# Performance work log

Hardware: AMD Instinct MI355X
Metric: run time of the kernel (lower is better)

The kernel has to match this reference:

```python
import jax, jax.numpy as jnp
from jax import lax
import numpy as np

T = 140
H = 64
B = 8192

def _uniform(key, shape, k):
    return jax.random.uniform(key, shape, dtype=jnp.float32, minval=-k, maxval=k)

def setup_inputs() -> dict:
    key = jax.random.key(0)
    ks = jax.random.split(key, 12)
    k = 1.0 / np.sqrt(H)  # torch default init bound
    return {
        "x": jax.random.normal(ks[0], (B, T, 1), dtype=jnp.float32),
        "h_state": jnp.zeros((2, B, H), dtype=jnp.float32),
        "W_ih0": _uniform(ks[1], (H, 1), k),
        "W_hh0": _uniform(ks[2], (H, H), k),
        "b_ih0": _uniform(ks[3], (H,), k),
        "b_hh0": _uniform(ks[4], (H,), k),
        "W_ih1": _uniform(ks[5], (H, H), k),
        "W_hh1": _uniform(ks[6], (H, H), k),
        "b_ih1": _uniform(ks[7], (H,), k),
        "b_hh1": _uniform(ks[8], (H,), k),
        "W_out": _uniform(ks[9], (1, H), k),
        "b_out": _uniform(ks[10], (1,), k),
    }

def reference(x, h_state, W_ih0, W_hh0, b_ih0, b_hh0, W_ih1, W_hh1, b_ih1, b_hh1, W_out, b_out):
    b = x.shape[0]
    x = x.reshape(b, T, 1)
    xs = jnp.swapaxes(x, 0, 1)  # [T, B, 1]

    def step(carry, xt):
        h0, h1 = carry
        # torch RNN cell: h_t = tanh(x W_ih^T + b_ih + h_{t-1} W_hh^T + b_hh)
        h0n = jnp.tanh(xt @ W_ih0.T + b_ih0 + h0 @ W_hh0.T + b_hh0)
        h1n = jnp.tanh(h0n @ W_ih1.T + b_ih1 + h1 @ W_hh1.T + b_hh1)
        return (h0n, h1n), h1n

    (hf0, hf1), ys = lax.scan(step, (h_state[0], h_state[1]), xs)
    ys = jnp.swapaxes(ys, 0, 1)  # [B, T, H]
    out = (ys @ W_out.T + b_out).reshape(b, T, 1)
    h_final = jnp.stack([hf0, hf1])  # [2, B, H]
    return out, h_final
```

## Files before the change

kernel.cpp:

```cpp
#include <hip/hip_runtime.h>

#define TT 140
#define BB 8192
#define HH 64
#define BT 16
#define WIN 4
#define K_TANH 2.88539008178f

typedef _Float16 half4 __attribute__((ext_vector_type(4)));
typedef float    f32x4 __attribute__((ext_vector_type(4)));

#define MFMA16(a,b,c) __builtin_amdgcn_mfma_f32_16x16x16f16(a, b, c, 0, 0, 0)

__device__ __forceinline__ float tanh_ps(float as) {
    float e = __builtin_amdgcn_exp2f(as);
    return 1.0f - 2.0f * __builtin_amdgcn_rcpf(e + 1.0f);
}

__device__ __forceinline__ half4 ldw4(const float* p, float s) {
    f32x4 w = *(const f32x4*)p;
    half4 h;
    #pragma unroll
    for (int i = 0; i < 4; ++i) h[i] = (_Float16)(s * w[i]);
    return h;
}

__global__ __launch_bounds__(128, 1)
void rnn_kernel(const float* __restrict__ x,
                const float* __restrict__ h_state,
                const float* __restrict__ W_ih0,
                const float* __restrict__ W_hh0,
                const float* __restrict__ b_ih0,
                const float* __restrict__ b_hh0,
                const float* __restrict__ W_ih1,
                const float* __restrict__ W_hh1,
                const float* __restrict__ b_ih1,
                const float* __restrict__ b_hh1,
                const float* __restrict__ W_out,
                const float* __restrict__ b_out,
                float* __restrict__ out)
{
    __shared__ float xs[TT * 17];
    __shared__ float pps[TT * 17];
    __shared__ f32x4 ei[2 * WIN][4][64];

    const int tid  = threadIdx.x;
    const int wid  = tid >> 6;
    const int lane = tid & 63;
    const int n    = lane & 15;
    const int q    = lane >> 4;
    const int b0   = blockIdx.x * BT;

    half4 A0[4][4], AI[4][4], AH[4][4];
    float e00[4][4], e10[4][4], e01[4][4], WO[4][4];
    half4 H0[4], H1[4];
    float bout = 0.f;
    if (wid == 0) {
        #pragma unroll
        for (int g = 0; g < 4; ++g)
        #pragma unroll
        for (int kk = 0; kk < 4; ++kk) {
            const int off = (16 * g + n) * HH + 16 * kk + 4 * q;
            A0[g][kk] = ldw4(W_hh0 + off, K_TANH);
            AI[g][kk] = ldw4(W_ih1 + off, K_TANH);
        }
        #pragma unroll
        for (int g = 0; g < 4; ++g)
        #pragma unroll
        for (int r = 0; r < 4; ++r) {
            int j = 16 * g + 4 * q + r;
            e00[g][r] = K_TANH * (b_ih0[j] + b_hh0[j]);
            e10[g][r] = K_TANH * W_ih0[j];
        }
        #pragma unroll
        for (int kk = 0; kk < 4; ++kk)
            H0[kk] = ldw4(h_state + (size_t)(b0 + n) * HH + 16 * kk + 4 * q, 1.0f);
    } else {
        #pragma unroll
        for (int g = 0; g < 4; ++g)
        #pragma unroll
        for (int kk = 0; kk < 4; ++kk) {
            const int off = (16 * g + n) * HH + 16 * kk + 4 * q;
            AH[g][kk] = ldw4(W_hh1 + off, K_TANH);
        }
        #pragma unroll
        for (int g = 0; g < 4; ++g)
        #pragma unroll
        for (int r = 0; r < 4; ++r) {
            int j = 16 * g + 4 * q + r;
            e01[g][r] = K_TANH * (b_ih1[j] + b_hh1[j]);
            WO[g][r]  = W_out[j];
        }
        #pragma unroll
        for (int kk = 0; kk < 4; ++kk)
            H1[kk] = ldw4(h_state + (size_t)BB * HH + (size_t)(b0 + n) * HH
                                   + 16 * kk + 4 * q, 1.0f);
        bout = b_out[0];
    }

    for (int i = tid; i < TT * BT; i += 128) {
        int t = i >> 4, b = i & 15;
        xs[t * 17 + b] = x[(size_t)(b0 + b) * TT + t];
    }
    __syncthreads();

    for (int win = 0; win <= TT / WIN; ++win) {
        if (wid == 0) {
            if (win < TT / WIN) {
                #pragma unroll
                for (int j = 0; j < WIN; ++j) {
                    const int p  = WIN * win + j;
                    const int pb = ((win & 1) ? WIN : 0) + j;
                    float xt = xs[p * 17 + n];
                    f32x4 d[4];
                    #pragma unroll
                    for (int g = 0; g < 4; ++g) {
                        f32x4 c;
                        #pragma unroll
                        for (int r = 0; r < 4; ++r) c[r] = e00[g][r] + e10[g][r] * xt;
                        #pragma unroll
                        for (int kk = 0; kk < 4; ++kk) c = MFMA16(A0[g][kk], H0[kk], c);
                        d[g] = c;
                    }
                    #pragma unroll
                    for (int g = 0; g < 4; ++g) {
                        half4 h;
                        #pragma unroll
                        for (int r = 0; r < 4; ++r) h[r] = (_Float16)tanh_ps(d[g][r]);
                        H0[g] = h;
                    }
                    #pragma unroll
                    for (int g = 0; g < 4; ++g) {
                        f32x4 c = {0.f, 0.f, 0.f, 0.f};
                        #pragma unroll
                        for (int kk = 0; kk < 4; ++kk) c = MFMA16(AI[g][kk], H0[kk], c);
                        ei[pb][g][lane] = c;
                    }
                }
            }
        } else {
            if (win >= 1) {
                #pragma unroll
                for (int j = 0; j < WIN; ++j) {
                    const int s  = WIN * (win - 1) + j;
                    const int sb = (((win - 1) & 1) ? WIN : 0) + j;
                    f32x4 d[4];
                    #pragma unroll
                    for (int g = 0; g < 4; ++g) {
                        f32x4 ep = ei[sb][g][lane];
                        f32x4 c;
                        #pragma unroll
                        for (int r = 0; r < 4; ++r) c[r] = e01[g][r] + ep[r];
                        #pragma unroll
                        for (int kk = 0; kk < 4; ++kk) c = MFMA16(AH[g][kk], H1[kk], c);
                        d[g] = c;
                    }
                    float pr = 0.f;
                    #pragma unroll
                    for (int g = 0; g < 4; ++g) {
                        half4 h;
                        #pragma unroll
                        for (int r = 0; r < 4; ++r) {
                            float hn = tanh_ps(d[g][r]);
                            pr += hn * WO[g][r];
                            h[r] = (_Float16)hn;
                        }
                        H1[g] = h;
                    }
                    pr += __shfl_xor(pr, 16, 64);
                    pr += __shfl_xor(pr, 32, 64);
                    if (lane < 16) pps[s * 17 + n] = pr + bout;
                }
            }
        }
        __syncthreads();
    }

    for (int i = tid; i < TT * BT; i += 128) {
        int t = i >> 4, b = i & 15;
        out[(size_t)(b0 + b) * TT + t] = pps[t * 17 + b];
    }
    const size_t OFF = (size_t)BB * TT;
    if (wid == 0) {
        #pragma unroll
        for (int kk = 0; kk < 4; ++kk) {
            f32x4 v;
            #pragma unroll
            for (int i = 0; i < 4; ++i) v[i] = (float)H0[kk][i];
            *(f32x4*)(out + OFF + (size_t)(b0 + n) * HH + 16 * kk + 4 * q) = v;
        }
    } else {
        #pragma unroll
        for (int kk = 0; kk < 4; ++kk) {
            f32x4 v;
            #pragma unroll
            for (int i = 0; i < 4; ++i) v[i] = (float)H1[kk][i];
            *(f32x4*)(out + OFF + (size_t)BB * HH + (size_t)(b0 + n) * HH
                               + 16 * kk + 4 * q) = v;
        }
    }
}

extern "C" void kernel_launch(void* const* d_in, const int* in_sizes, int n_in,
                              void* d_out, int out_size, void* d_ws, size_t ws_size,
                              hipStream_t stream) {
    const float* x      = (const float*)d_in[0];
    const float* hst    = (const float*)d_in[1];
    const float* W_ih0  = (const float*)d_in[2];
    const float* W_hh0  = (const float*)d_in[3];
    const float* b_ih0  = (const float*)d_in[4];
    const float* b_hh0  = (const float*)d_in[5];
    const float* W_ih1  = (const float*)d_in[6];
    const float* W_hh1  = (const float*)d_in[7];
    const float* b_ih1  = (const float*)d_in[8];
    const float* b_hh1  = (const float*)d_in[9];
    const float* W_out  = (const float*)d_in[10];
    const float* b_outp = (const float*)d_in[11];
    float* out = (float*)d_out;

    dim3 grid(BB / BT);
    dim3 block(128);
    rnn_kernel<<<grid, block, 0, stream>>>(x, hst, W_ih0, W_hh0, b_ih0, b_hh0,
                                           W_ih1, W_hh1, b_ih1, b_hh1,
                                           W_out, b_outp, out);
}
```

Before: 170.8 us.

## Switch recurrent matmuls to 16x16x32 f16 MFMA with bpermute state redistribution

Replaces the 16x16x16 f16 MFMA chains (four per output group) with the 16x16x32 instruction available on this architecture, halving the number of MFMA issues per step. Because the K=32 operand layout no longer matches the accumulator layout, the new hidden state is packed to half2 and reshuffled across lanes with ds_bpermute before the next step. This trades serial MFMA latency on the recurrence critical path for extra cross-lane permute traffic.

```diff
diff --git a/kernel.cpp b/kernel.cpp
--- a/kernel.cpp
+++ b/kernel.cpp
@@ -7,22 +7,53 @@
 #define WIN 4
 #define K_TANH 2.88539008178f
 
-typedef _Float16 half4 __attribute__((ext_vector_type(4)));
-typedef float    f32x4 __attribute__((ext_vector_type(4)));
-
-#define MFMA16(a,b,c) __builtin_amdgcn_mfma_f32_16x16x16f16(a, b, c, 0, 0, 0)
+typedef _Float16 half8  __attribute__((ext_vector_type(8)));
+typedef _Float16 half2v __attribute__((ext_vector_type(2)));
+typedef float    f32x4  __attribute__((ext_vector_type(4)));
+typedef int      int4v  __attribute__((ext_vector_type(4)));
+
+#define MFMA32(a,b,c) __builtin_amdgcn_mfma_f32_16x16x32_f16(a, b, c, 0, 0, 0)
 
 __device__ __forceinline__ float tanh_ps(float as) {
     float e = __builtin_amdgcn_exp2f(as);
     return 1.0f - 2.0f * __builtin_amdgcn_rcpf(e + 1.0f);
 }
 
-__device__ __forceinline__ half4 ldw4(const float* p, float s) {
-    f32x4 w = *(const f32x4*)p;
-    half4 h;
+__device__ __forceinline__ half8 ldw8(const float* p, float s) {
+    f32x4 a = *(const f32x4*)p;
+    f32x4 b = *(const f32x4*)(p + 4);
+    half8 h;
     #pragma unroll
-    for (int i = 0; i < 4; ++i) h[i] = (_Float16)(s * w[i]);
+    for (int j = 0; j < 8; ++j) h[j] = (_Float16)(s * ((j < 4) ? a[j] : b[j - 4]));
     return h;
+}
+
+__device__ __forceinline__ int pack2(float a, float b) {
+    half2v h; h[0] = (_Float16)a; h[1] = (_Float16)b;
+    union { half2v h; int i; } u; u.h = h; return u.i;
+}
+
+__device__ __forceinline__ void redist(const float th[4][4], int idxA, int idxB,
+                                       bool hiq, half8 H[2]) {
+    int P[4][2];
+    #pragma unroll
+    for (int g = 0; g < 4; ++g) {
+        P[g][0] = pack2(th[g][0], th[g][1]);
+        P[g][1] = pack2(th[g][2], th[g][3]);
+    }
+    #pragma unroll
+    for (int kt = 0; kt < 2; ++kt) {
+        int a0 = __builtin_amdgcn_ds_bpermute(idxA, P[2 * kt][0]);
+        int b0 = __builtin_amdgcn_ds_bpermute(idxA, P[2 * kt + 1][0]);
+        int a1 = __builtin_amdgcn_ds_bpermute(idxA, P[2 * kt][1]);
+        int b1 = __builtin_amdgcn_ds_bpermute(idxA, P[2 * kt + 1][1]);
+        int a2 = __builtin_amdgcn_ds_bpermute(idxB, P[2 * kt][0]);
+        int b2 = __builtin_amdgcn_ds_bpermute(idxB, P[2 * kt + 1][0]);
+        int a3 = __builtin_amdgcn_ds_bpermute(idxB, P[2 * kt][1]);
+        int b3 = __builtin_amdgcn_ds_bpermute(idxB, P[2 * kt + 1][1]);
+        int4v w = { hiq ? b0 : a0, hiq ? b1 : a1, hiq ? b2 : a2, hiq ? b3 : a3 };
+        union { int4v w; half8 h; } u; u.w = w; H[kt] = u.h;
+    }
 }
 
 __global__ __launch_bounds__(128, 1)
@@ -51,18 +82,22 @@
     const int q    = lane >> 4;
     const int b0   = blockIdx.x * BT;
 
-    half4 A0[4][4], AI[4][4], AH[4][4];
+    const int idxA = (((2 * q) & 3) * 16 + n) * 4;
+    const int idxB = (((2 * q + 1) & 3) * 16 + n) * 4;
+    const bool hiq = (q >= 2);
+
+    half8 A0[4][2], AI[4][2], AH[4][2];
     float e00[4][4], e10[4][4], e01[4][4], WO[4][4];
-    half4 H0[4], H1[4];
+    half8 H0[2], H1[2];
     float bout = 0.f;
     if (wid == 0) {
         #pragma unroll
         for (int g = 0; g < 4; ++g)
         #pragma unroll
-        for (int kk = 0; kk < 4; ++kk) {
-            const int off = (16 * g + n) * HH + 16 * kk + 4 * q;
-            A0[g][kk] = ldw4(W_hh0 + off, K_TANH);
-            AI[g][kk] = ldw4(W_ih1 + off, K_TANH);
+        for (int kt = 0; kt < 2; ++kt) {
+            const int off = (16 * g + n) * HH + 32 * kt + 8 * q;
+            A0[g][kt] = ldw8(W_hh0 + off, K_TANH);
+            AI[g][kt] = ldw8(W_ih1 + off, K_TANH);
         }
         #pragma unroll
         for (int g = 0; g < 4; ++g)
@@ -73,15 +108,15 @@
             e10[g][r] = K_TANH * W_ih0[j];
         }
         #pragma unroll
-        for (int kk = 0; kk < 4; ++kk)
-            H0[kk] = ldw4(h_state + (size_t)(b0 + n) * HH + 16 * kk + 4 * q, 1.0f);
+        for (int kt = 0; kt < 2; ++kt)
+            H0[kt] = ldw8(h_state + (size_t)(b0 + n) * HH + 32 * kt + 8 * q, 1.0f);
     } else {
         #pragma unroll
         for (int g = 0; g < 4; ++g)
         #pragma unroll
-        for (int kk = 0; kk < 4; ++kk) {
-            const int off = (16 * g + n) * HH + 16 * kk + 4 * q;
-            AH[g][kk] = ldw4(W_hh1 + off, K_TANH);
+        for (int kt = 0; kt < 2; ++kt) {
+            const int off = (16 * g + n) * HH + 32 * kt + 8 * q;
+            AH[g][kt] = ldw8(W_hh1 + off, K_TANH);
         }
         #pragma unroll
         for (int g = 0; g < 4; ++g)
@@ -92,9 +127,9 @@
             WO[g][r]  = W_out[j];
         }
         #pragma unroll
-        for (int kk = 0; kk < 4; ++kk)
-            H1[kk] = ldw4(h_state + (size_t)BB * HH + (size_t)(b0 + n) * HH
-                                   + 16 * kk + 4 * q, 1.0f);
+        for (int kt = 0; kt < 2; ++kt)
+            H1[kt] = ldw8(h_state + (size_t)BB * HH + (size_t)(b0 + n) * HH
+                                   + 32 * kt + 8 * q, 1.0f);
         bout = b_out[0];
     }
 
@@ -112,28 +147,23 @@
                     const int p  = WIN * win + j;
                     const int pb = ((win & 1) ? WIN : 0) + j;
                     float xt = xs[p * 17 + n];
-                    f32x4 d[4];
+                    float th[4][4];
                     #pragma unroll
                     for (int g = 0; g < 4; ++g) {
                         f32x4 c;
                         #pragma unroll
                         for (int r = 0; r < 4; ++r) c[r] = e00[g][r] + e10[g][r] * xt;
-                        #pragma unroll
-                        for (int kk = 0; kk < 4; ++kk) c = MFMA16(A0[g][kk], H0[kk], c);
-                        d[g] = c;
+                        c = MFMA32(A0[g][0], H0[0], c);
+                        c = MFMA32(A0[g][1], H0[1], c);
+                        #pragma unroll
+                        for (int r = 0; r < 4; ++r) th[g][r] = tanh_ps(c[r]);
                     }
-                    #pragma unroll
-                    for (int g = 0; g < 4; ++g) {
-                        half4 h;
-                        #pragma unroll
-                        for (int r = 0; r < 4; ++r) h[r] = (_Float16)tanh_ps(d[g][r]);
-                        H0[g] = h;
-                    }
+                    redist(th, idxA, idxB, hiq, H0);
                     #pragma unroll
                     for (int g = 0; g < 4; ++g) {
                         f32x4 c = {0.f, 0.f, 0.f, 0.f};
-                        #pragma unroll
-                        for (int kk = 0; kk < 4; ++kk) c = MFMA16(AI[g][kk], H0[kk], c);
+                        c = MFMA32(AI[g][0], H0[0], c);
+                        c = MFMA32(AI[g][1], H0[1], c);
                         ei[pb][g][lane] = c;
                     }
                 }
@@ -144,29 +174,24 @@
                 for (int j = 0; j < WIN; ++j) {
                     const int s  = WIN * (win - 1) + j;
                     const int sb = (((win - 1) & 1) ? WIN : 0) + j;
-                    f32x4 d[4];
+                    float th[4][4];
+                    float pr = 0.f;
                     #pragma unroll
                     for (int g = 0; g < 4; ++g) {
                         f32x4 ep = ei[sb][g][lane];
                         f32x4 c;
                         #pragma unroll
                         for (int r = 0; r < 4; ++r) c[r] = e01[g][r] + ep[r];
-                        #pragma unroll
-                        for (int kk = 0; kk < 4; ++kk) c = MFMA16(AH[g][kk], H1[kk], c);
-                        d[g] = c;
+                        c = MFMA32(AH[g][0], H1[0], c);
+                        c = MFMA32(AH[g][1], H1[1], c);
+                        #pragma unroll
+                        for (int r = 0; r < 4; ++r) {
+                            float hn = tanh_ps(c[r]);
+                            th[g][r] = hn;
+                            pr += hn * WO[g][r];
+                        }
                     }
-                    float pr = 0.f;
-                    #pragma unroll
-                    for (int g = 0; g < 4; ++g) {
-                        half4 h;
-                        #pragma unroll
-                        for (int r = 0; r < 4; ++r) {
-                            float hn = tanh_ps(d[g][r]);
-                            pr += hn * WO[g][r];
-                            h[r] = (_Float16)hn;
-                        }
-                        H1[g] = h;
-                    }
+                    redist(th, idxA, idxB, hiq, H1);
                     pr += __shfl_xor(pr, 16, 64);
                     pr += __shfl_xor(pr, 32, 64);
                     if (lane < 16) pps[s * 17 + n] = pr + bout;
@@ -183,21 +208,17 @@
     const size_t OFF = (size_t)BB * TT;
     if (wid == 0) {
         #pragma unroll
-        for (int kk = 0; kk < 4; ++kk) {
-            f32x4 v;
-            #pragma unroll
-            for (int i = 0; i < 4; ++i) v[i] = (float)H0[kk][i];
-            *(f32x4*)(out + OFF + (size_t)(b0 + n) * HH + 16 * kk + 4 * q) = v;
-        }
+        for (int kt = 0; kt < 2; ++kt)
+        #pragma unroll
+        for (int j = 0; j < 8; ++j)
+            out[OFF + (size_t)(b0 + n) * HH + 32 * kt + 8 * q + j] = (float)H0[kt][j];
     } else {
         #pragma unroll
-        for (int kk = 0; kk < 4; ++kk) {
-            f32x4 v;
-            #pragma unroll
-            for (int i = 0; i < 4; ++i) v[i] = (float)H1[kk][i];
-            *(f32x4*)(out + OFF + (size_t)BB * HH + (size_t)(b0 + n) * HH
-                               + 16 * kk + 4 * q) = v;
-        }
+        for (int kt = 0; kt < 2; ++kt)
+        #pragma unroll
+        for (int j = 0; j < 8; ++j)
+            out[OFF + (size_t)BB * HH + (size_t)(b0 + n) * HH + 32 * kt + 8 * q + j]
+                = (float)H1[kt][j];
     }
 }
 
```

Result: slower. 211.0 us (+23.5%).
